# Performance work log

Hardware: AMD Instinct MI355X
Metric: run time of the kernel (lower is better)

Reference implementation:

```python
import jax, jax.numpy as jnp
import numpy as np

EMBED_DIM = 768
NUM_HEADS = 12


def setup_inputs() -> dict:
    key = jax.random.key(0)
    k_x, k_w1, k_b1, k_w2, k_b2 = jax.random.split(key, 5)
    B, S, D = 4, 2048, EMBED_DIM
    s1 = 1.0 / np.sqrt(D)
    return {
        "x": jax.random.normal(k_x, (B, S, D), dtype=jnp.float32),
        "W1": jax.random.uniform(k_w1, (D, 3 * D), jnp.float32, -s1, s1),  # proj1 weight (in,out)
        "b1": jax.random.uniform(k_b1, (3 * D,), jnp.float32, -s1, s1),
        "W2": jax.random.uniform(k_w2, (D, D), jnp.float32, -s1, s1),  # proj2 weight (in,out)
        "b2": jax.random.uniform(k_b2, (D,), jnp.float32, -s1, s1),
    }


def reference(x, W1, b1, W2, b2):
    B, S, D = x.shape
    H = NUM_HEADS
    h = D // H
    qkv = x @ W1 + b1                       # [B,S,3D]
    qkv = qkv.reshape(B, S, H, 3 * h).transpose(0, 2, 1, 3)  # [B,H,S,3h]
    # chunk order in the original: K, Q, V
    K = qkv[..., :h]
    Q = qkv[..., h:2 * h]
    V = qkv[..., 2 * h:]
    # NOTE: original code computes Q @ V^T (not Q @ K^T) -- reproduced faithfully
    scores = jnp.einsum("bhqd,bhkd->bhqk", Q, V) / jnp.sqrt(jnp.float32(h))
    att = jax.nn.softmax(scores, axis=-1)
    out = jnp.einsum("bhqk,bhkd->bhqd", att, V)  # [B,H,S,h]
    out = out.transpose(0, 2, 1, 3).reshape(B, S, D)
    return out @ W2 + b2
```

## Files before the change

### kernel.cpp

```cpp
#include <hip/hip_runtime.h>
#include <hip/hip_bf16.h>
#include <math.h>


#define SEQ   2048
#define DIM   768
#define NHEAD 12
#define HDIM  64
#define BATCH 4

#define QSCALE 0.1803368801111244f

typedef __attribute__((ext_vector_type(8))) short s16x8;
typedef __attribute__((ext_vector_type(4))) float f32x4;

#if __has_builtin(__builtin_amdgcn_exp2f)
#define EXP2F(x) __builtin_amdgcn_exp2f(x)
#else
#define EXP2F(x) exp2f(x)
#endif

__device__ __forceinline__ unsigned short f2bf(float f) {
    union { float f; unsigned int u; } v; v.f = f;
    unsigned int r = v.u + 0x7fffu + ((v.u >> 16) & 1u);
    return (unsigned short)(r >> 16);
}

__device__ __forceinline__ void gload_lds16(const void* g, void* l) {
    __builtin_amdgcn_global_load_lds(
        (const __attribute__((address_space(1))) unsigned int*)g,
        (__attribute__((address_space(3))) unsigned int*)l, 16, 0, 0);
}

__global__ __launch_bounds__(256) void cvt_x(const float* __restrict__ x,
                                             unsigned short* __restrict__ xb)
{
    const size_t i4 = ((size_t)blockIdx.x * 256 + threadIdx.x) * 4;
    float4 v = *(const float4*)&x[i4];
    ushort4 o;
    o.x = f2bf(v.x); o.y = f2bf(v.y); o.z = f2bf(v.z); o.w = f2bf(v.w);
    *(ushort4*)&xb[i4] = o;
}

__global__ __launch_bounds__(256) void cvt_wt(const float* __restrict__ W,
                                              unsigned short* __restrict__ out,
                                              int src_ld, int qvmap)
{
    __shared__ float T[32][33];
    const int n0 = blockIdx.x * 32, k0 = blockIdx.y * 32;
    const int c0 = qvmap ? ((n0 >> 7) * 192 + 64 + (n0 & 127)) : n0;
    const int tc = threadIdx.x & 31, tr = threadIdx.x >> 5;
    #pragma unroll
    for (int i = 0; i < 4; ++i)
        T[tr + i * 8][tc] = W[(size_t)(k0 + tr + i * 8) * src_ld + c0 + tc];
    __syncthreads();
    #pragma unroll
    for (int i = 0; i < 4; ++i)
        out[(size_t)(n0 + tr + i * 8) * DIM + k0 + tc] = f2bf(T[tc][tr + i * 8]);
}

__device__ __forceinline__ void gemm128_loop(
    const unsigned short* __restrict__ A, const unsigned short* __restrict__ B,
    unsigned short* As, unsigned short* Bs, int m0, int n0, f32x4 acc[4][4])
{
    const int tid  = threadIdx.x;
    const int wave = tid >> 6;
    const int lane = tid & 63;
    const int quad = lane >> 4;
    const int lcol = lane & 15;
    const int wm = wave >> 1, wn = wave & 1;

    const int sr = lane >> 2;
    const int sp = lane & 3;
    const int sc = sp ^ ((sr >> 1) & 3);

    const int aswz = ((quad ^ ((lcol >> 1) & 3)) << 4);

    for (int k0 = 0; k0 < DIM; k0 += 32) {
        #pragma unroll
        for (int s = 0; s < 2; ++s) {
            const int r0 = wave * 32 + s * 16;
            gload_lds16(&A[(size_t)(m0 + r0 + sr) * DIM + k0 + sc * 8],
                        (void*)&As[r0 * 32]);
            gload_lds16(&B[(size_t)(n0 + r0 + sr) * DIM + k0 + sc * 8],
                        (void*)&Bs[r0 * 32]);
        }
        __syncthreads();

        s16x8 af[4], bf[4];
        #pragma unroll
        for (int mt = 0; mt < 4; ++mt) {
            const int row = wm * 64 + mt * 16 + lcol;
            af[mt] = *(const s16x8*)((const char*)As + row * 64 + aswz);
        }
        #pragma unroll
        for (int nt = 0; nt < 4; ++nt) {
            const int row = wn * 64 + nt * 16 + lcol;
            bf[nt] = *(const s16x8*)((const char*)Bs + row * 64 + aswz);
        }
        #pragma unroll
        for (int mt = 0; mt < 4; ++mt)
            #pragma unroll
            for (int nt = 0; nt < 4; ++nt)
                acc[mt][nt] = __builtin_amdgcn_mfma_f32_16x16x32_bf16(
                    af[mt], bf[nt], acc[mt][nt], 0, 0, 0);
        __syncthreads();
    }
}

__global__ __launch_bounds__(256) void qkv_gemm_bf16(
    const unsigned short* __restrict__ xb, const unsigned short* __restrict__ W1bt,
    const float* __restrict__ b1, unsigned short* __restrict__ Qb,
    unsigned short* __restrict__ Vr, unsigned short* __restrict__ Vt)
{
    __shared__ unsigned short LDSBUF[8192];
    f32x4 acc[4][4] = {};
    const int m0 = blockIdx.y * 128, n0 = blockIdx.x * 128;
    gemm128_loop(xb, W1bt, LDSBUF, LDSBUF + 4096, m0, n0, acc);

    const int tid  = threadIdx.x;
    const int wave = tid >> 6, lane = tid & 63;
    const int quad = lane >> 4, lcol = lane & 15;
    const int wm = wave >> 1, wn = wave & 1;

    const int colblock = n0 + wn * 64;
    const int head = colblock >> 7;
    const int cc0  = colblock & 127;
    const int isQ  = (cc0 == 0);
    const float scale = isQ ? QSCALE : 1.0f;
    unsigned short* dst = isQ ? Qb : Vr;

    float bias[4];
    #pragma unroll
    for (int nt = 0; nt < 4; ++nt)
        bias[nt] = b1[head * 192 + 64 + cc0 + nt * 16 + lcol];

    unsigned short* Wst = LDSBUF + wave * 2048;

    #pragma unroll
    for (int half = 0; half < 2; ++half) {
        #pragma unroll
        for (int mh = 0; mh < 2; ++mh) {
            const int mt = half * 2 + mh;
            #pragma unroll
            for (int nt = 0; nt < 4; ++nt)
                #pragma unroll
                for (int r = 0; r < 4; ++r) {
                    const float v = (acc[mt][nt][r] + bias[nt]) * scale;
                    Wst[(mh * 16 + quad * 4 + r) * 64 + nt * 16 + lcol] = f2bf(v);
                }
        }
        __syncthreads();
        #pragma unroll
        for (int p = 0; p < 4; ++p) {
            const int lr = p * 8 + (lane >> 3);
            const int c8 = (lane & 7) * 8;
            s16x8 v = *(const s16x8*)&Wst[lr * 64 + c8];
            const int m  = m0 + wm * 64 + half * 32 + lr;
            const int bb = m >> 11;
            const int s  = m & 2047;
            const int bhh = bb * NHEAD + head;
            *(s16x8*)&dst[((size_t)bhh * SEQ + s) * HDIM + c8] = v;
        }
        __syncthreads();
    }

    if (!isQ) {
        #pragma unroll
        for (int nt = 0; nt < 4; ++nt) {
            const int d = nt * 16 + lcol;
            #pragma unroll
            for (int mt = 0; mt < 4; ++mt) {
                const int m0r = m0 + wm * 64 + mt * 16 + quad * 4;
                const int bb  = m0r >> 11;
                const int s0  = m0r & 2047;
                const int bhh = bb * NHEAD + head;
                ushort4 o;
                o.x = f2bf(acc[mt][nt][0] + bias[nt]);
                o.y = f2bf(acc[mt][nt][1] + bias[nt]);
                o.z = f2bf(acc[mt][nt][2] + bias[nt]);
                o.w = f2bf(acc[mt][nt][3] + bias[nt]);
                *(ushort4*)&Vt[((size_t)bhh * HDIM + d) * SEQ + s0] = o;
            }
        }
    }
}

__global__ __launch_bounds__(256) void attn_mfma(
    const unsigned short* __restrict__ Qb, const unsigned short* __restrict__ Vr,
    const unsigned short* __restrict__ Vt, unsigned short* __restrict__ Yb)
{
    __shared__ unsigned short VrS[64 * 64];
    __shared__ unsigned short VtS[64 * 64];
    __shared__ unsigned short Ps[4][32 * 72];

    const int bh = blockIdx.y;
    const int b  = bh / NHEAD;
    const int hh = bh % NHEAD;
    const int q0 = blockIdx.x * 128;

    const int tid  = threadIdx.x;
    const int wave = tid >> 6;
    const int lane = tid & 63;
    const int quad = lane >> 4;
    const int lcol = lane & 15;

    s16x8 qa[2][2];
    #pragma unroll
    for (int mt = 0; mt < 2; ++mt)
        #pragma unroll
        for (int kk = 0; kk < 2; ++kk)
            qa[mt][kk] = *(const s16x8*)&Qb[((size_t)bh * SEQ + q0 + wave * 32 + mt * 16 + lcol) * HDIM
                                            + kk * 32 + quad * 8];

    s16x8 ones;
    #pragma unroll
    for (int i = 0; i < 8; ++i) ones[i] = (short)0x3F80;

    f32x4 oacc[2][4] = {};
    f32x4 lsum[2] = {};

    const int srow = lane >> 3;
    const int schk = (lane & 7) ^ srow;

    for (int k0 = 0; k0 < SEQ; k0 += 64) {
        #pragma unroll
        for (int s = 0; s < 2; ++s) {
            const int r0 = wave * 16 + s * 8;
            gload_lds16(&Vr[((size_t)bh * SEQ + k0 + r0 + srow) * HDIM + schk * 8],
                        (void*)&VrS[r0 * 64]);
            gload_lds16(&Vt[((size_t)bh * HDIM + r0 + srow) * SEQ + k0 + schk * 8],
                        (void*)&VtS[r0 * 64]);
        }
        __syncthreads();

        f32x4 sacc[2][4] = {};
        #pragma unroll
        for (int kk = 0; kk < 2; ++kk) {
            s16x8 bf[4];
            #pragma unroll
            for (int nt = 0; nt < 4; ++nt) {
                const int r = nt * 16 + lcol;
                const int c = kk * 4 + quad;
                bf[nt] = *(const s16x8*)((const char*)VrS + r * 128 + ((c ^ (r & 7)) << 4));
            }
            #pragma unroll
            for (int mt = 0; mt < 2; ++mt)
                #pragma unroll
                for (int nt = 0; nt < 4; ++nt)
                    sacc[mt][nt] = __builtin_amdgcn_mfma_f32_16x16x32_bf16(
                        qa[mt][kk], bf[nt], sacc[mt][nt], 0, 0, 0);
        }

        #pragma unroll
        for (int mt = 0; mt < 2; ++mt)
            #pragma unroll
            for (int nt = 0; nt < 4; ++nt)
                #pragma unroll
                for (int r = 0; r < 4; ++r) {
                    const float p = EXP2F(sacc[mt][nt][r]);
                    Ps[wave][(mt * 16 + quad * 4 + r) * 72 + nt * 16 + lcol] = f2bf(p);
                }

        #pragma unroll
        for (int kk = 0; kk < 2; ++kk) {
            s16x8 pa[2];
            #pragma unroll
            for (int mt = 0; mt < 2; ++mt)
                pa[mt] = *(const s16x8*)&Ps[wave][(mt * 16 + lcol) * 72 + kk * 32 + quad * 8];
            #pragma unroll
            for (int mt = 0; mt < 2; ++mt)
                lsum[mt] = __builtin_amdgcn_mfma_f32_16x16x32_bf16(
                    pa[mt], ones, lsum[mt], 0, 0, 0);
            #pragma unroll
            for (int dt = 0; dt < 4; ++dt) {
                const int r = dt * 16 + lcol;
                const int c = kk * 4 + quad;
                s16x8 vb = *(const s16x8*)((const char*)VtS + r * 128 + ((c ^ (r & 7)) << 4));
                #pragma unroll
                for (int mt = 0; mt < 2; ++mt)
                    oacc[mt][dt] = __builtin_amdgcn_mfma_f32_16x16x32_bf16(
                        pa[mt], vb, oacc[mt][dt], 0, 0, 0);
            }
        }
        __syncthreads();
    }

    #pragma unroll
    for (int mt = 0; mt < 2; ++mt)
        #pragma unroll
        for (int r = 0; r < 4; ++r) {
            const float invl = 1.0f / lsum[mt][r];
            const int qrow = q0 + wave * 32 + mt * 16 + quad * 4 + r;
            #pragma unroll
            for (int dt = 0; dt < 4; ++dt)
                Yb[((size_t)b * SEQ + qrow) * DIM + hh * HDIM + dt * 16 + lcol] =
                    f2bf(oacc[mt][dt][r] * invl);
        }
}

__global__ __launch_bounds__(256) void proj_gemm_bf16(
    const unsigned short* __restrict__ Yb, const unsigned short* __restrict__ W2bt,
    const float* __restrict__ b2, float* __restrict__ out)
{
    __shared__ unsigned short LDSBUF[8192];
    f32x4 acc[4][4] = {};
    const int m0 = blockIdx.y * 128, n0 = blockIdx.x * 128;
    gemm128_loop(Yb, W2bt, LDSBUF, LDSBUF + 4096, m0, n0, acc);

    const int tid  = threadIdx.x;
    const int wave = tid >> 6, lane = tid & 63;
    const int quad = lane >> 4, lcol = lane & 15;
    const int wm = wave >> 1, wn = wave & 1;

    float bias[4];
    #pragma unroll
    for (int nt = 0; nt < 4; ++nt)
        bias[nt] = b2[n0 + wn * 64 + nt * 16 + lcol];

    float* W32 = (float*)LDSBUF + wave * 1024;

    #pragma unroll
    for (int mt = 0; mt < 4; ++mt) {
        #pragma unroll
        for (int nt = 0; nt < 4; ++nt)
            #pragma unroll
            for (int r = 0; r < 4; ++r)
                W32[(quad * 4 + r) * 64 + nt * 16 + lcol] = acc[mt][nt][r] + bias[nt];
        __syncthreads();
        #pragma unroll
        for (int p = 0; p < 4; ++p) {
            const int lr = p * 4 + (lane >> 4);
            float4 v = *(const float4*)&W32[lr * 64 + (lane & 15) * 4];
            const int m = m0 + wm * 64 + mt * 16 + lr;
            *(float4*)&out[(size_t)m * DIM + n0 + wn * 64 + (lane & 15) * 4] = v;
        }
        __syncthreads();
    }
}

extern "C" void kernel_launch(void* const* d_in, const int* in_sizes, int n_in,
                              void* d_out, int out_size, void* d_ws, size_t ws_size,
                              hipStream_t stream)
{
    const float* x  = (const float*)d_in[0];
    const float* W1 = (const float*)d_in[1];
    const float* b1 = (const float*)d_in[2];
    const float* W2 = (const float*)d_in[3];
    const float* b2 = (const float*)d_in[4];
    float* out = (float*)d_out;

    const size_t NQV = (size_t)BATCH * NHEAD * SEQ * HDIM;
    unsigned short* Qb   = (unsigned short*)d_ws;
    unsigned short* Vr   = Qb + NQV;
    unsigned short* Vt   = Vr + NQV;
    unsigned short* Yb   = Vt + NQV;
    unsigned short* xb   = Yb + NQV;
    unsigned short* W1bt = xb + NQV;
    unsigned short* W2bt = W1bt + 1536 * DIM;

    cvt_x <<<6144, 256, 0, stream>>>(x, xb);
    cvt_wt<<<dim3(48, 24), 256, 0, stream>>>(W1, W1bt, 2304, 1);
    cvt_wt<<<dim3(24, 24), 256, 0, stream>>>(W2, W2bt, DIM, 0);

    qkv_gemm_bf16<<<dim3(12, 64), 256, 0, stream>>>(xb, W1bt, b1, Qb, Vr, Vt);
    attn_mfma<<<dim3(SEQ / 128, BATCH * NHEAD), 256, 0, stream>>>(Qb, Vr, Vt, Yb);
    proj_gemm_bf16<<<dim3(6, 64), 256, 0, stream>>>(Yb, W2bt, b2, out);
}
```

Measured before the change: 220.9 us.

## Transpose score MFMA for packed P stores and shrink proj GEMM tile

In attention, the score MFMA operands are swapped so each lane holds four consecutive keys for one query row. The probabilities can then be packed to bf16 pairs and written to LDS as 8-byte stores instead of scalar 16-bit stores. The output projection GEMM switches from 128x128 to 64x128 tiles with its own K-loop, doubling the block count from 384 to 768 for better CU fill. The new loop has no double buffering, so a sync stall comes at every k-step.

Result: slower. 250.0 us (+13.2%).

```diff
diff --git a/kernel.cpp b/kernel.cpp
--- a/kernel.cpp
+++ b/kernel.cpp
@@ -24,6 +24,16 @@
     union { float f; unsigned int u; } v; v.f = f;
     unsigned int r = v.u + 0x7fffu + ((v.u >> 16) & 1u);
     return (unsigned short)(r >> 16);
+}
+
+__device__ __forceinline__ unsigned int pk2bf(float a, float b) {
+#if __has_builtin(__builtin_amdgcn_cvt_pk_bf16_f32)
+    typedef __attribute__((ext_vector_type(2))) __bf16 bf16x2;
+    bf16x2 v = __builtin_amdgcn_cvt_pk_bf16_f32(a, b);
+    return __builtin_bit_cast(unsigned int, v);
+#else
+    return (unsigned int)f2bf(a) | ((unsigned int)f2bf(b) << 16);
+#endif
 }
 
 __device__ __forceinline__ void gload_lds16(const void* g, void* l) {
@@ -234,33 +244,37 @@
         }
         __syncthreads();
 
-        f32x4 sacc[2][4] = {};
+        f32x4 saccT[2][4] = {};
         #pragma unroll
         for (int kk = 0; kk < 2; ++kk) {
-            s16x8 bf[4];
-            #pragma unroll
-            for (int nt = 0; nt < 4; ++nt) {
-                const int r = nt * 16 + lcol;
+            s16x8 vf[4];
+            #pragma unroll
+            for (int st = 0; st < 4; ++st) {
+                const int r = st * 16 + lcol;
                 const int c = kk * 4 + quad;
-                bf[nt] = *(const s16x8*)((const char*)VrS + r * 128 + ((c ^ (r & 7)) << 4));
+                vf[st] = *(const s16x8*)((const char*)VrS + r * 128 + ((c ^ (r & 7)) << 4));
             }
             #pragma unroll
             for (int mt = 0; mt < 2; ++mt)
                 #pragma unroll
-                for (int nt = 0; nt < 4; ++nt)
-                    sacc[mt][nt] = __builtin_amdgcn_mfma_f32_16x16x32_bf16(
-                        qa[mt][kk], bf[nt], sacc[mt][nt], 0, 0, 0);
+                for (int st = 0; st < 4; ++st)
+                    saccT[mt][st] = __builtin_amdgcn_mfma_f32_16x16x32_bf16(
+                        vf[st], qa[mt][kk], saccT[mt][st], 0, 0, 0);
         }
 
         #pragma unroll
         for (int mt = 0; mt < 2; ++mt)
             #pragma unroll
-            for (int nt = 0; nt < 4; ++nt)
-                #pragma unroll
-                for (int r = 0; r < 4; ++r) {
-                    const float p = EXP2F(sacc[mt][nt][r]);
-                    Ps[wave][(mt * 16 + quad * 4 + r) * 72 + nt * 16 + lcol] = f2bf(p);
-                }
+            for (int st = 0; st < 4; ++st) {
+                const float p0 = EXP2F(saccT[mt][st][0]);
+                const float p1 = EXP2F(saccT[mt][st][1]);
+                const float p2 = EXP2F(saccT[mt][st][2]);
+                const float p3 = EXP2F(saccT[mt][st][3]);
+                uint2 u;
+                u.x = pk2bf(p0, p1);
+                u.y = pk2bf(p2, p3);
+                *(uint2*)&Ps[wave][(mt * 16 + lcol) * 72 + st * 16 + quad * 4] = u;
+            }
 
         #pragma unroll
         for (int kk = 0; kk < 2; ++kk) {
@@ -304,14 +318,58 @@
     const float* __restrict__ b2, float* __restrict__ out)
 {
     __shared__ unsigned short LDSBUF[8192];
-    f32x4 acc[4][4] = {};
-    const int m0 = blockIdx.y * 128, n0 = blockIdx.x * 128;
-    gemm128_loop(Yb, W2bt, LDSBUF, LDSBUF + 4096, m0, n0, acc);
+    unsigned short* As = LDSBUF;
+    unsigned short* Bs = LDSBUF + 2048;
 
     const int tid  = threadIdx.x;
-    const int wave = tid >> 6, lane = tid & 63;
-    const int quad = lane >> 4, lcol = lane & 15;
+    const int wave = tid >> 6;
+    const int lane = tid & 63;
+    const int quad = lane >> 4;
+    const int lcol = lane & 15;
     const int wm = wave >> 1, wn = wave & 1;
+
+    const int m0 = blockIdx.y * 64, n0 = blockIdx.x * 128;
+
+    const int sr = lane >> 2;
+    const int sp = lane & 3;
+    const int sc = sp ^ ((sr >> 1) & 3);
+    const int aswz = ((quad ^ ((lcol >> 1) & 3)) << 4);
+
+    f32x4 acc[2][4] = {};
+
+    for (int k0 = 0; k0 < DIM; k0 += 32) {
+        {
+            const int r0 = wave * 16;
+            gload_lds16(&Yb[(size_t)(m0 + r0 + sr) * DIM + k0 + sc * 8],
+                        (void*)&As[r0 * 32]);
+        }
+        #pragma unroll
+        for (int s = 0; s < 2; ++s) {
+            const int r0 = wave * 32 + s * 16;
+            gload_lds16(&W2bt[(size_t)(n0 + r0 + sr) * DIM + k0 + sc * 8],
+                        (void*)&Bs[r0 * 32]);
+        }
+        __syncthreads();
+
+        s16x8 af[2], bf[4];
+        #pragma unroll
+        for (int mt = 0; mt < 2; ++mt) {
+            const int row = wm * 32 + mt * 16 + lcol;
+            af[mt] = *(const s16x8*)((const char*)As + row * 64 + aswz);
+        }
+        #pragma unroll
+        for (int nt = 0; nt < 4; ++nt) {
+            const int row = wn * 64 + nt * 16 + lcol;
+            bf[nt] = *(const s16x8*)((const char*)Bs + row * 64 + aswz);
+        }
+        #pragma unroll
+        for (int mt = 0; mt < 2; ++mt)
+            #pragma unroll
+            for (int nt = 0; nt < 4; ++nt)
+                acc[mt][nt] = __builtin_amdgcn_mfma_f32_16x16x32_bf16(
+                    af[mt], bf[nt], acc[mt][nt], 0, 0, 0);
+        __syncthreads();
+    }
 
     float bias[4];
     #pragma unroll
@@ -321,7 +379,7 @@
     float* W32 = (float*)LDSBUF + wave * 1024;
 
     #pragma unroll
-    for (int mt = 0; mt < 4; ++mt) {
+    for (int mt = 0; mt < 2; ++mt) {
         #pragma unroll
         for (int nt = 0; nt < 4; ++nt)
             #pragma unroll
@@ -332,7 +390,7 @@
         for (int p = 0; p < 4; ++p) {
             const int lr = p * 4 + (lane >> 4);
             float4 v = *(const float4*)&W32[lr * 64 + (lane & 15) * 4];
-            const int m = m0 + wm * 64 + mt * 16 + lr;
+            const int m = m0 + wm * 32 + mt * 16 + lr;
             *(float4*)&out[(size_t)m * DIM + n0 + wn * 64 + (lane & 15) * 4] = v;
         }
         __syncthreads();
@@ -365,5 +423,5 @@
 
     qkv_gemm_bf16<<<dim3(12, 64), 256, 0, stream>>>(xb, W1bt, b1, Qb, Vr, Vt);
     attn_mfma<<<dim3(SEQ / 128, BATCH * NHEAD), 256, 0, stream>>>(Qb, Vr, Vt, Yb);
-    proj_gemm_bf16<<<dim3(6, 64), 256, 0, stream>>>(Yb, W2bt, b2, out);
-}
+    proj_gemm_bf16<<<dim3(DIM / 128, 128), 256, 0, stream>>>(Yb, W2bt, b2, out);
+}
```
